# Performance work log

Hardware: AMD Instinct MI355X
Metric: run time of the kernel (lower is better)

## Reference

```python
import jax, jax.numpy as jnp
import numpy as np

INV_SQRT_2 = 0.7071067811865476


def setup_inputs() -> dict:
    key = jax.random.key(0)
    k1, k2, k3, k4, k5 = jax.random.split(key, 5)
    batch, nodes, edges, dim_in, dim_out = 2, 10000, 320000, 64, 64
    x = jax.random.normal(k1, (batch, nodes, dim_in, 3), dtype=jnp.float32)
    src = jax.random.randint(k2, (edges,), 0, nodes, dtype=jnp.int32)
    dst = jax.random.randint(k3, (edges,), 0, nodes, dtype=jnp.int32)
    # VecLinear weights (no bias; equivariant linear over the channel dim)
    W_src = jax.random.normal(k4, (dim_out, dim_in), dtype=jnp.float32) / np.sqrt(dim_in)
    W_dst = jax.random.normal(k5, (dim_out, dim_in), dtype=jnp.float32) / np.sqrt(dim_in)
    return {"x": x, "W_src": W_src, "W_dst": W_dst, "src": src, "dst": dst}


def reference(x, W_src, W_dst, src, dst):
    # x: (b, nodes, dim_in, 3); gather node feats per edge, mix channels, combine.
    xs = jnp.take(x, src, axis=1)  # (b, edges, dim_in, 3)
    xd = jnp.take(x, dst, axis=1)  # (b, edges, dim_in, 3)
    ys = jnp.einsum('oi,beiv->beov', W_src, xs)
    yd = jnp.einsum('oi,beiv->beov', W_dst, xd)
    return (ys + yd) * INV_SQRT_2  # (b, edges, dim_out, 3)
```

## Files before the change

### kernel.cpp

```cpp
#include <hip/hip_runtime.h>

#define INV_SQRT_2F 0.70710678118654752440f

typedef float fvec4 __attribute__((ext_vector_type(4)));

static __device__ __forceinline__ unsigned short f2bf(float f)
{
    unsigned int u = __float_as_uint(f);
    u += 0x7fffu + ((u >> 16) & 1u);
    return (unsigned short)(u >> 16);
}

static __device__ __forceinline__ fvec4 combine4(uint2 a, uint2 b)
{
    fvec4 r;
    r.x = (__uint_as_float(a.x << 16)         + __uint_as_float(b.x << 16))         * INV_SQRT_2F;
    r.y = (__uint_as_float(a.x & 0xffff0000u) + __uint_as_float(b.x & 0xffff0000u)) * INV_SQRT_2F;
    r.z = (__uint_as_float(a.y << 16)         + __uint_as_float(b.y << 16))         * INV_SQRT_2F;
    r.w = (__uint_as_float(a.y & 0xffff0000u) + __uint_as_float(b.y & 0xffff0000u)) * INV_SQRT_2F;
    return r;
}

__global__ void pack_sd(const int* __restrict__ src,
                        const int* __restrict__ dst,
                        unsigned int* __restrict__ sd, int edges)
{
    int i = blockIdx.x * blockDim.x + threadIdx.x;
    int stride = gridDim.x * blockDim.x;
    for (; i < edges; i += stride)
        sd[i] = ((unsigned int)src[i] << 16) | (unsigned int)dst[i];
}

__global__ void __launch_bounds__(128)
node_transform(const float* __restrict__ x,
               const float* __restrict__ W_src,
               const float* __restrict__ W_dst,
               unsigned short* __restrict__ y_src,
               unsigned short* __restrict__ y_dst,
               int nodes, int bn_total)
{
    __shared__ float xs[192];
    int bn = blockIdx.x;
    if (bn >= bn_total) return;
    int b = bn / nodes;
    int n = bn - b * nodes;

    const float4* xp = (const float4*)(x + (size_t)bn * 192);
    int t = threadIdx.x;
    if (t < 48) ((float4*)xs)[t] = xp[t];
    __syncthreads();

    int o = t & 63;
    const float*    W = (t < 64) ? W_src : W_dst;
    unsigned short* y = (t < 64) ? y_src : y_dst;

    const float4* Wrow = (const float4*)(W + o * 64);
    float a0 = 0.f, a1 = 0.f, a2 = 0.f;
#pragma unroll
    for (int i4 = 0; i4 < 16; ++i4) {
        float4 w = Wrow[i4];
        int i = i4 * 4;
        a0 = fmaf(w.x, xs[(i + 0) * 3 + 0], a0);
        a1 = fmaf(w.x, xs[(i + 0) * 3 + 1], a1);
        a2 = fmaf(w.x, xs[(i + 0) * 3 + 2], a2);
        a0 = fmaf(w.y, xs[(i + 1) * 3 + 0], a0);
        a1 = fmaf(w.y, xs[(i + 1) * 3 + 1], a1);
        a2 = fmaf(w.y, xs[(i + 1) * 3 + 2], a2);
        a0 = fmaf(w.z, xs[(i + 2) * 3 + 0], a0);
        a1 = fmaf(w.z, xs[(i + 2) * 3 + 1], a1);
        a2 = fmaf(w.z, xs[(i + 2) * 3 + 2], a2);
        a0 = fmaf(w.w, xs[(i + 3) * 3 + 0], a0);
        a1 = fmaf(w.w, xs[(i + 3) * 3 + 1], a1);
        a2 = fmaf(w.w, xs[(i + 3) * 3 + 2], a2);
    }
    int h = o >> 5;
    int c = o & 31;
    unsigned short* yp = y + (((size_t)(b * 2 + h) * nodes + n) * 96) + c * 3;
    yp[0] = f2bf(a0);
    yp[1] = f2bf(a1);
    yp[2] = f2bf(a2);
}

__global__ void __launch_bounds__(256)
edge_combine_phased(const unsigned short* __restrict__ y_src,
                    const unsigned short* __restrict__ y_dst,
                    const unsigned int* __restrict__ sd,
                    float* __restrict__ out,
                    int edges, int nodes)
{
    const int total  = edges * 96;
    const int stride = gridDim.x * blockDim.x;
    const uint2* ys = (const uint2*)y_src;
    const uint2* yd = (const uint2*)y_dst;
    fvec4*       o4 = (fvec4*)out;

    for (int t = blockIdx.x * blockDim.x + threadIdx.x; t < total; t += stride) {
        int pe = t / 24;
        int j  = t - pe * 24;
        int p  = pe / edges;
        int e  = pe - p * edges;

        unsigned int q = __builtin_nontemporal_load(&sd[e]);
        unsigned int srow = q >> 16;
        unsigned int drow = q & 0xffffu;

        uint2 a = ys[((size_t)p * nodes + srow) * 24 + j];
        uint2 b = yd[((size_t)p * nodes + drow) * 24 + j];

        int bb = p >> 1;
        int h  = p & 1;
        size_t ob = ((size_t)bb * edges + e) * 48 + h * 24 + j;
        __builtin_nontemporal_store(combine4(a, b), &o4[ob]);
    }
}

__global__ void __launch_bounds__(256)
edge_combine_phased_u(const unsigned short* __restrict__ y_src,
                      const unsigned short* __restrict__ y_dst,
                      const int* __restrict__ src,
                      const int* __restrict__ dst,
                      float* __restrict__ out,
                      int edges, int nodes)
{
    const int total  = edges * 96;
    const int stride = gridDim.x * blockDim.x;
    const uint2* ys = (const uint2*)y_src;
    const uint2* yd = (const uint2*)y_dst;
    fvec4*       o4 = (fvec4*)out;

    for (int t = blockIdx.x * blockDim.x + threadIdx.x; t < total; t += stride) {
        int pe = t / 24;
        int j  = t - pe * 24;
        int p  = pe / edges;
        int e  = pe - p * edges;

        unsigned int srow = (unsigned int)__builtin_nontemporal_load(&src[e]);
        unsigned int drow = (unsigned int)__builtin_nontemporal_load(&dst[e]);

        uint2 a = ys[((size_t)p * nodes + srow) * 24 + j];
        uint2 b = yd[((size_t)p * nodes + drow) * 24 + j];

        int bb = p >> 1;
        int h  = p & 1;
        size_t ob = ((size_t)bb * edges + e) * 48 + h * 24 + j;
        __builtin_nontemporal_store(combine4(a, b), &o4[ob]);
    }
}

__global__ void __launch_bounds__(64)
edge_fused(const float* __restrict__ x,
           const float* __restrict__ W_src,
           const float* __restrict__ W_dst,
           const int* __restrict__ src,
           const int* __restrict__ dst,
           float* __restrict__ out,
           int edges, int nodes)
{
    __shared__ float xs[192];
    __shared__ float xd[192];
    int be = blockIdx.x;
    int b  = be / edges;
    int e  = be - b * edges;
    int s  = src[e];
    int d  = dst[e];
    const float* xps = x + ((size_t)b * nodes + s) * 192;
    const float* xpd = x + ((size_t)b * nodes + d) * 192;
    int t = threadIdx.x;
#pragma unroll
    for (int k = 0; k < 3; ++k) {
        xs[t + 64 * k] = xps[t + 64 * k];
        xd[t + 64 * k] = xpd[t + 64 * k];
    }
    __syncthreads();
    float a0 = 0.f, a1 = 0.f, a2 = 0.f;
#pragma unroll
    for (int i = 0; i < 64; ++i) {
        float ws = W_src[t * 64 + i];
        float wd = W_dst[t * 64 + i];
        a0 += ws * xs[i * 3 + 0] + wd * xd[i * 3 + 0];
        a1 += ws * xs[i * 3 + 1] + wd * xd[i * 3 + 1];
        a2 += ws * xs[i * 3 + 2] + wd * xd[i * 3 + 2];
    }
    float* op = out + ((size_t)b * edges + e) * 192 + t * 3;
    op[0] = a0 * INV_SQRT_2F;
    op[1] = a1 * INV_SQRT_2F;
    op[2] = a2 * INV_SQRT_2F;
}

extern "C" void kernel_launch(void* const* d_in, const int* in_sizes, int n_in,
                              void* d_out, int out_size, void* d_ws, size_t ws_size,
                              hipStream_t stream)
{
    const float* x     = (const float*)d_in[0];
    const float* W_src = (const float*)d_in[1];
    const float* W_dst = (const float*)d_in[2];
    const int*   src   = (const int*)d_in[3];
    const int*   dst   = (const int*)d_in[4];
    float*       out   = (float*)d_out;

    const int batch = 2;
    const int edges = in_sizes[3];
    const int nodes = in_sizes[0] / (batch * 192);

    const size_t y_elems = (size_t)batch * nodes * 192;
    const size_t y_bytes = ((y_elems * 2 + 255) / 256) * 256;
    const size_t sd_bytes = (((size_t)edges * 4 + 255) / 256) * 256;
    const size_t needed_packed = 2 * y_bytes + sd_bytes;
    const size_t needed_plain  = 2 * y_bytes;

    char* wsb = (char*)d_ws;
    const int bn_total = batch * nodes;

    if (ws_size >= needed_packed && nodes <= 65535) {
        unsigned short* y_src = (unsigned short*)wsb;
        unsigned short* y_dst = (unsigned short*)(wsb + y_bytes);
        unsigned int*   sd    = (unsigned int*)(wsb + 2 * y_bytes);

        node_transform<<<bn_total, 128, 0, stream>>>(x, W_src, W_dst,
                                                     y_src, y_dst, nodes, bn_total);
        int egrid = (edges + 255) / 256; if (egrid > 1024) egrid = 1024;
        pack_sd<<<egrid, 256, 0, stream>>>(src, dst, sd, edges);
        edge_combine_phased<<<2048, 256, 0, stream>>>(y_src, y_dst, sd, out,
                                                      edges, nodes);
    } else if (ws_size >= needed_plain) {
        unsigned short* y_src = (unsigned short*)wsb;
        unsigned short* y_dst = (unsigned short*)(wsb + y_bytes);
        node_transform<<<bn_total, 128, 0, stream>>>(x, W_src, W_dst,
                                                     y_src, y_dst, nodes, bn_total);
        edge_combine_phased_u<<<2048, 256, 0, stream>>>(y_src, y_dst, src, dst,
                                                        out, edges, nodes);
    } else {
        edge_fused<<<batch * edges, 64, 0, stream>>>(x, W_src, W_dst,
                                                     src, dst, out, edges, nodes);
    }
}
```

Measured before the change: 251.1 us.

## Pin each phase of edge combine to an XCD pair for L2 locality

```diff
diff --git a/kernel.cpp b/kernel.cpp
--- a/kernel.cpp
+++ b/kernel.cpp
@@ -82,33 +82,39 @@
 }
 
 __global__ void __launch_bounds__(256)
-edge_combine_phased(const unsigned short* __restrict__ y_src,
-                    const unsigned short* __restrict__ y_dst,
-                    const unsigned int* __restrict__ sd,
-                    float* __restrict__ out,
-                    int edges, int nodes)
-{
-    const int total  = edges * 96;
-    const int stride = gridDim.x * blockDim.x;
+edge_combine_xcd(const unsigned short* __restrict__ y_src,
+                 const unsigned short* __restrict__ y_dst,
+                 const unsigned int* __restrict__ sd,
+                 float* __restrict__ out,
+                 int edges, int nodes)
+{
     const uint2* ys = (const uint2*)y_src;
     const uint2* yd = (const uint2*)y_dst;
     fvec4*       o4 = (fvec4*)out;
 
-    for (int t = blockIdx.x * blockDim.x + threadIdx.x; t < total; t += stride) {
-        int pe = t / 24;
-        int j  = t - pe * 24;
-        int p  = pe / edges;
-        int e  = pe - p * edges;
+    int bid  = blockIdx.x;
+    int xcd  = bid & 7;
+    int p    = xcd & 3;
+    int rep  = bid >> 3;
+    int half = xcd >> 2;
+    int nrep = (int)(gridDim.x >> 3);
+    int tid  = ((rep * 2 + half) * (int)blockDim.x) + (int)threadIdx.x;
+    int nthr = nrep * 2 * (int)blockDim.x;
+
+    const uint2* ysp = ys + (size_t)p * nodes * 24;
+    const uint2* ydp = yd + (size_t)p * nodes * 24;
+    const int bb = p >> 1;
+    const int h  = p & 1;
+    const int total = edges * 24;
+
+    for (int t = tid; t < total; t += nthr) {
+        int e = t / 24;
+        int j = t - e * 24;
 
         unsigned int q = __builtin_nontemporal_load(&sd[e]);
-        unsigned int srow = q >> 16;
-        unsigned int drow = q & 0xffffu;
-
-        uint2 a = ys[((size_t)p * nodes + srow) * 24 + j];
-        uint2 b = yd[((size_t)p * nodes + drow) * 24 + j];
-
-        int bb = p >> 1;
-        int h  = p & 1;
+        uint2 a = ysp[(size_t)(q >> 16)     * 24 + j];
+        uint2 b = ydp[(size_t)(q & 0xffffu) * 24 + j];
+
         size_t ob = ((size_t)bb * edges + e) * 48 + h * 24 + j;
         __builtin_nontemporal_store(combine4(a, b), &o4[ob]);
     }
@@ -220,8 +226,8 @@
                                                      y_src, y_dst, nodes, bn_total);
         int egrid = (edges + 255) / 256; if (egrid > 1024) egrid = 1024;
         pack_sd<<<egrid, 256, 0, stream>>>(src, dst, sd, edges);
-        edge_combine_phased<<<2048, 256, 0, stream>>>(y_src, y_dst, sd, out,
-                                                      edges, nodes);
+        edge_combine_xcd<<<2048, 256, 0, stream>>>(y_src, y_dst, sd, out,
+                                                   edges, nodes);
     } else if (ws_size >= needed_plain) {
         unsigned short* y_src = (unsigned short*)wsb;
         unsigned short* y_dst = (unsigned short*)(wsb + y_bytes);
```

Measured after the change: 249.8 us. Within noise of the previous version (-0.5%).
